# Kernel optimization log

Measured on AMD Instinct MI355X. Metric: run time of the kernel, lower is better.

The kernel has to match this reference:

```python
import jax, jax.numpy as jnp
import numpy as np


def setup_inputs() -> dict:
    key = jax.random.key(0)
    kq, kk, kv = jax.random.split(key, 3)
    B, H, S, D = 1, 16, 4096, 64
    Q = jax.random.normal(kq, (B, H, S, D), dtype=jnp.float32)
    K = jax.random.normal(kk, (B, H, S, D), dtype=jnp.float32)
    V = jax.random.normal(kv, (B, H, S, D), dtype=jnp.float32)
    return {"Q": Q, "K": K, "V": V}


def reference(Q, K, V):
    # scores: [B, H, len_q, len_k], scaled by sqrt(dim_k)
    dim_k = K.shape[-1]
    scale = 1.0 / jnp.sqrt(jnp.asarray(dim_k, dtype=Q.dtype))
    scores = jnp.einsum("bhqd,bhkd->bhqk", Q, K) * scale
    attention = jax.nn.softmax(scores, axis=-1)
    context = jnp.einsum("bhqk,bhkd->bhqd", attention, V)
    return context
```

## Files before the change

kernel.cpp:

```cpp
#include <hip/hip_runtime.h>
#include <hip/hip_bf16.h>

typedef short bf16x8 __attribute__((ext_vector_type(8)));
typedef __bf16 bfv8  __attribute__((ext_vector_type(8)));
typedef __bf16 bfv4  __attribute__((ext_vector_type(4)));
typedef float f32x4  __attribute__((ext_vector_type(4)));

#define S_LEN 4096
#define DDIM  64
#define KVB   32
#define QBLK  128
#define NHEAD 16
#define THR   7.0f
#define VOFFB 4096
#define BUFSZ 9216

#define MFMA(a, b, c) __builtin_amdgcn_mfma_f32_16x16x32_bf16((a), (b), (c), 0, 0, 0)

static __device__ __forceinline__ float exp2v(float x) {
    return __builtin_amdgcn_exp2f(x);
}

static __device__ __forceinline__ int4 cvt8(float4 a, float4 b) {
    bfv8 r;
    r[0] = (__bf16)a.x; r[1] = (__bf16)a.y; r[2] = (__bf16)a.z; r[3] = (__bf16)a.w;
    r[4] = (__bf16)b.x; r[5] = (__bf16)b.y; r[6] = (__bf16)b.z; r[7] = (__bf16)b.w;
    return __builtin_bit_cast(int4, r);
}
static __device__ __forceinline__ int2 cvt4(f32x4 a) {
    bfv4 r;
    r[0] = (__bf16)a[0]; r[1] = (__bf16)a[1]; r[2] = (__bf16)a[2]; r[3] = (__bf16)a[3];
    return __builtin_bit_cast(int2, r);
}

static __device__ __forceinline__ bf16x8 ldfrag(const unsigned char* base, int row, int doff) {
    int addr = (row * 128 + doff * 2) ^ ((row & 7) << 4);
    return *reinterpret_cast<const bf16x8*>(base + addr);
}

static __device__ __forceinline__ void stage(unsigned char* base, int swK, int swV,
                                             float4 ka, float4 kb, int4 vt) {
    *reinterpret_cast<int4*>(base + swK)         = cvt8(ka, kb);
    *reinterpret_cast<int4*>(base + VOFFB + swV) = vt;
}

static __device__ __forceinline__ bf16x8 softmax_pb(f32x4 s0, f32x4 s1, float& m,
                                                    f32x4 acc[4], f32x4& lacc) {
    float mx = fmaxf(fmaxf(fmaxf(s0[0], s0[1]), s0[2]),
                     fmaxf(fmaxf(s0[3], s1[0]),
                           fmaxf(s1[1], fmaxf(s1[2], s1[3]))));
    if (!__all(mx <= m + THR)) {
        float pm = fmaxf(mx, __shfl_xor(mx, 16));
        pm = fmaxf(pm, __shfl_xor(pm, 32));
        float mn = fmaxf(m, pm);
        float al = exp2v(m - mn);
        #pragma unroll
        for (int dk = 0; dk < 4; ++dk)
            #pragma unroll
            for (int j = 0; j < 4; ++j) acc[dk][j] *= al;
        #pragma unroll
        for (int j = 0; j < 4; ++j) lacc[j] *= al;
        m = mn;
    }
    bfv8 r;
    #pragma unroll
    for (int j = 0; j < 4; ++j) {
        r[2 * j]     = (__bf16)exp2v(s0[j] - m);
        r[2 * j + 1] = (__bf16)exp2v(s1[j] - m);
    }
    return __builtin_bit_cast(bf16x8, r);
}

__global__ __launch_bounds__(256) void transpose_v(
    const float* __restrict__ Vg, unsigned short* __restrict__ wsVT)
{
    const int h  = blockIdx.y;
    const int kt = blockIdx.x;
    const int t  = threadIdx.x;
    __shared__ __align__(16) unsigned short vt[32][68];

    {
        const int key = t >> 3;
        const int d0  = (t & 7) * 8;
        const float* vp = Vg + (((size_t)h * S_LEN) + (size_t)kt * 32 + key) * DDIM + d0;
        float4 a = *reinterpret_cast<const float4*>(vp);
        float4 b = *reinterpret_cast<const float4*>(vp + 4);
        int4 w = cvt8(a, b);
        int2 lo = {w.x, w.y}, hi = {w.z, w.w};
        *reinterpret_cast<int2*>(&vt[key][d0])     = lo;
        *reinterpret_cast<int2*>(&vt[key][d0 + 4]) = hi;
    }
    __syncthreads();
    {
        const int d  = t >> 2;
        const int p0 = (t & 3) * 8;
        unsigned short out[8];
        #pragma unroll
        for (int i = 0; i < 8; ++i) {
            int p   = p0 + i;
            int key = 4 * (p >> 3) + ((p & 7) >> 1) + 16 * (p & 1);
            out[i] = vt[key][d];
        }
        size_t off = (((size_t)h * DDIM + d) * 128 + kt) * 32 + p0;
        *reinterpret_cast<int4*>(wsVT + off) = *reinterpret_cast<const int4*>(out);
    }
}

template <int KSPLIT>
__global__ __launch_bounds__(256, 3) void attn_fwd(
    const float* __restrict__ Qg, const float* __restrict__ Kg,
    const unsigned short* __restrict__ wsVT, float* __restrict__ Og,
    unsigned short* __restrict__ wsO, float* __restrict__ wsML)
{
    const int h    = blockIdx.y;
    const int qb   = blockIdx.x;
    const int ks   = (KSPLIT > 1) ? blockIdx.z : 0;
    const int NT   = (S_LEN / KVB) / KSPLIT;
    const int tid  = threadIdx.x;
    const int lane = tid & 63;
    const int wv   = tid >> 6;
    const int g    = lane >> 4;
    const int r16  = lane & 15;

    __shared__ __align__(16) unsigned char lds[2 * BUFSZ];

    const float QSC = 0.125f * 1.44269504088896f;
    const int qrow0 = qb * QBLK + wv * 32 + r16;
    bf16x8 qf0[2], qf1[2];
    {
        const float* qp0 = Qg + ((size_t)h * S_LEN + qrow0) * DDIM;
        const float* qp1 = qp0 + 16 * DDIM;
        #pragma unroll
        for (int c = 0; c < 2; ++c) {
            float4 x = *reinterpret_cast<const float4*>(qp0 + 32 * c + 8 * g);
            float4 y = *reinterpret_cast<const float4*>(qp0 + 32 * c + 8 * g + 4);
            float4 xs = {x.x * QSC, x.y * QSC, x.z * QSC, x.w * QSC};
            float4 ys = {y.x * QSC, y.y * QSC, y.z * QSC, y.w * QSC};
            qf0[c] = __builtin_bit_cast(bf16x8, cvt8(xs, ys));
            x = *reinterpret_cast<const float4*>(qp1 + 32 * c + 8 * g);
            y = *reinterpret_cast<const float4*>(qp1 + 32 * c + 8 * g + 4);
            xs = {x.x * QSC, x.y * QSC, x.z * QSC, x.w * QSC};
            ys = {y.x * QSC, y.y * QSC, y.z * QSC, y.w * QSC};
            qf1[c] = __builtin_bit_cast(bf16x8, cvt8(xs, ys));
        }
    }

    bf16x8 ones;
    #pragma unroll
    for (int e = 0; e < 8; ++e) ones[e] = (short)0x3F80;

    const int srow = tid >> 3;
    const int sd   = (tid & 7) * 8;
    const int swK  = (srow * 128 + sd * 2) ^ ((srow & 7) << 4);
    const int vrow = tid >> 2;
    const int swV  = vrow * 80 + (tid & 3) * 16;

    const float* kp = Kg + (size_t)h * S_LEN * DDIM
                    + (size_t)ks * (S_LEN / KSPLIT) * DDIM
                    + (size_t)srow * DDIM + sd;
    const unsigned short* vtp = wsVT
        + (((size_t)h * DDIM + vrow) * 128 + (size_t)ks * (128 / KSPLIT)) * 32
        + (tid & 3) * 8;

    float4 ka = *reinterpret_cast<const float4*>(kp);
    float4 kb = *reinterpret_cast<const float4*>(kp + 4);
    int4   vt = *reinterpret_cast<const int4*>(vtp);
    stage(lds, swK, swV, ka, kb, vt);
    kp += KVB * DDIM; vtp += 32;
    ka = *reinterpret_cast<const float4*>(kp);
    kb = *reinterpret_cast<const float4*>(kp + 4);
    vt = *reinterpret_cast<const int4*>(vtp);
    __syncthreads();

    const f32x4 z0 = {0.f, 0.f, 0.f, 0.f};
    f32x4 accA[4] = {z0, z0, z0, z0};
    f32x4 accB[4] = {z0, z0, z0, z0};
    f32x4 laccA = z0, laccB = z0;
    float m0 = -INFINITY, m1 = -INFINITY;

    int c = 0;
    for (int kt = 0; kt < NT; ++kt) {
        const unsigned char* Klds = lds + c * BUFSZ;
        const unsigned char* Vlds = Klds + VOFFB;

        if (kt + 1 < NT) {
            stage(lds + (c ^ 1) * BUFSZ, swK, swV, ka, kb, vt);
            if (kt + 2 < NT) {
                kp += KVB * DDIM; vtp += 32;
                ka = *reinterpret_cast<const float4*>(kp);
                kb = *reinterpret_cast<const float4*>(kp + 4);
                vt = *reinterpret_cast<const int4*>(vtp);
            }
        }

        bf16x8 vf[4];
        {
            const unsigned char* vbase = Vlds + r16 * 80 + 16 * g;
            #pragma unroll
            for (int dk = 0; dk < 4; ++dk)
                vf[dk] = *reinterpret_cast<const bf16x8*>(vbase + dk * 1280);
        }

        f32x4 sA0 = z0, sA1 = z0, sB0 = z0, sB1 = z0;
        #pragma unroll
        for (int cc = 0; cc < 2; ++cc) {
            bf16x8 k0 = ldfrag(Klds, r16,      32 * cc + 8 * g);
            bf16x8 k1 = ldfrag(Klds, 16 + r16, 32 * cc + 8 * g);
            sA0 = MFMA(k0, qf0[cc], sA0);
            sA1 = MFMA(k1, qf0[cc], sA1);
            sB0 = MFMA(k0, qf1[cc], sB0);
            sB1 = MFMA(k1, qf1[cc], sB1);
        }

        bf16x8 pbA = softmax_pb(sA0, sA1, m0, accA, laccA);
        bf16x8 pbB = softmax_pb(sB0, sB1, m1, accB, laccB);

        laccA = MFMA(ones, pbA, laccA);
        #pragma unroll
        for (int dk = 0; dk < 4; ++dk) accA[dk] = MFMA(vf[dk], pbA, accA[dk]);
        laccB = MFMA(ones, pbB, laccB);
        #pragma unroll
        for (int dk = 0; dk < 4; ++dk) accB[dk] = MFMA(vf[dk], pbB, accB[dk]);

        __syncthreads();
        c ^= 1;
    }

    if (KSPLIT == 1) {
        float inv0 = 1.0f / laccA[0];
        float* op = Og + ((size_t)h * S_LEN + qrow0) * DDIM;
        #pragma unroll
        for (int dk = 0; dk < 4; ++dk) {
            float4 o = {accA[dk][0] * inv0, accA[dk][1] * inv0,
                        accA[dk][2] * inv0, accA[dk][3] * inv0};
            *reinterpret_cast<float4*>(op + 16 * dk + 4 * g) = o;
        }
        float inv1 = 1.0f / laccB[0];
        op += 16 * DDIM;
        #pragma unroll
        for (int dk = 0; dk < 4; ++dk) {
            float4 o = {accB[dk][0] * inv1, accB[dk][1] * inv1,
                        accB[dk][2] * inv1, accB[dk][3] * inv1};
            *reinterpret_cast<float4*>(op + 16 * dk + 4 * g) = o;
        }
    } else {
        const size_t R0 = (size_t)h * S_LEN + qrow0;
        unsigned short* o0 = wsO + ((size_t)ks * (NHEAD * S_LEN) + R0) * DDIM;
        #pragma unroll
        for (int dk = 0; dk < 4; ++dk)
            *reinterpret_cast<int2*>(o0 + 16 * dk + 4 * g) = cvt4(accA[dk]);
        o0 += 16 * DDIM;
        #pragma unroll
        for (int dk = 0; dk < 4; ++dk)
            *reinterpret_cast<int2*>(o0 + 16 * dk + 4 * g) = cvt4(accB[dk]);
        if (g == 0) {
            float2 v0 = {m0, laccA[0]};
            float2 v1 = {m1, laccB[0]};
            *reinterpret_cast<float2*>(wsML + ((size_t)ks * (NHEAD * S_LEN) + R0) * 2)      = v0;
            *reinterpret_cast<float2*>(wsML + ((size_t)ks * (NHEAD * S_LEN) + R0 + 16) * 2) = v1;
        }
    }
}

__global__ __launch_bounds__(256) void combine2(
    const unsigned short* __restrict__ wsO, const float* __restrict__ wsML,
    float* __restrict__ Og)
{
    const int NR = NHEAD * S_LEN;
    int t  = blockIdx.x * 256 + threadIdx.x;
    int R  = t >> 4;
    int d4 = (t & 15) * 4;
    float2 ml0 = *reinterpret_cast<const float2*>(wsML + (size_t)R * 2);
    float2 ml1 = *reinterpret_cast<const float2*>(wsML + ((size_t)NR + R) * 2);
    float m  = fmaxf(ml0.x, ml1.x);
    float a0 = exp2v(ml0.x - m);
    float a1 = exp2v(ml1.x - m);
    float inv = 1.0f / (a0 * ml0.y + a1 * ml1.y);
    a0 *= inv; a1 *= inv;
    bfv4 o0 = __builtin_bit_cast(bfv4,
        *reinterpret_cast<const int2*>(wsO + (size_t)R * DDIM + d4));
    bfv4 o1 = __builtin_bit_cast(bfv4,
        *reinterpret_cast<const int2*>(wsO + ((size_t)NR + R) * DDIM + d4));
    float4 o = {a0 * (float)o0[0] + a1 * (float)o1[0],
                a0 * (float)o0[1] + a1 * (float)o1[1],
                a0 * (float)o0[2] + a1 * (float)o1[2],
                a0 * (float)o0[3] + a1 * (float)o1[3]};
    *reinterpret_cast<float4*>(Og + (size_t)R * DDIM + d4) = o;
}

extern "C" void kernel_launch(void* const* d_in, const int* in_sizes, int n_in,
                              void* d_out, int out_size, void* d_ws, size_t ws_size,
                              hipStream_t stream) {
    const float* Q = (const float*)d_in[0];
    const float* K = (const float*)d_in[1];
    const float* V = (const float*)d_in[2];
    float* O = (float*)d_out;

    const size_t nVT = (size_t)NHEAD * DDIM * S_LEN;
    const size_t nO  = (size_t)2 * NHEAD * S_LEN * DDIM;
    const size_t nML = (size_t)2 * NHEAD * S_LEN * 2;
    const size_t needVT   = nVT * 2;
    const size_t needFull = nVT * 2 + nO * 2 + nML * 4;

    unsigned short* wsVT = (unsigned short*)d_ws;
    transpose_v<<<dim3(128, NHEAD), dim3(256, 1, 1), 0, stream>>>(V, wsVT);

    if (ws_size >= needFull) {
        unsigned short* wsO  = wsVT + nVT;
        float*          wsML = (float*)(wsO + nO);
        dim3 grid(S_LEN / QBLK, NHEAD, 2);
        attn_fwd<2><<<grid, dim3(256, 1, 1), 0, stream>>>(Q, K, wsVT, O, wsO, wsML);
        int nthr = NHEAD * S_LEN * (DDIM / 4);
        combine2<<<dim3(nthr / 256), dim3(256, 1, 1), 0, stream>>>(wsO, wsML, O);
    } else if (ws_size >= needVT) {
        dim3 grid(S_LEN / QBLK, NHEAD, 1);
        attn_fwd<1><<<grid, dim3(256, 1, 1), 0, stream>>>(Q, K, wsVT, O, nullptr, nullptr);
    }
}
```

Before: 102.7 us.

## Pre-convert K to swizzled bf16 tiles and split keys three ways

K is now converted to bf16 once in a prep kernel and written as pre-swizzled 4KB tiles, so the attention kernel loads one int4 per thread and copies it straight into LDS. Previously every query block reloaded and converted fp32 K. The V transpose layout is also made tile-contiguous. The key split grows from 2 to 3 (43/43/42 tiles) to put more blocks on the device, and the combine kernel is generalized to N splits. The cost is a larger workspace, an extra K pass in the prep kernel, and more partial-output traffic in the combine.

```diff
diff --git a/kernel.cpp b/kernel.cpp
--- a/kernel.cpp
+++ b/kernel.cpp
@@ -38,10 +38,10 @@
     return *reinterpret_cast<const bf16x8*>(base + addr);
 }
 
-static __device__ __forceinline__ void stage(unsigned char* base, int swK, int swV,
-                                             float4 ka, float4 kb, int4 vt) {
-    *reinterpret_cast<int4*>(base + swK)         = cvt8(ka, kb);
-    *reinterpret_cast<int4*>(base + VOFFB + swV) = vt;
+static __device__ __forceinline__ void stage(unsigned char* base, int kdst, int vdst,
+                                             int4 kv, int4 vv) {
+    *reinterpret_cast<int4*>(base + kdst)         = kv;
+    *reinterpret_cast<int4*>(base + VOFFB + vdst) = vv;
 }
 
 static __device__ __forceinline__ bf16x8 softmax_pb(f32x4 s0, f32x4 s1, float& m,
@@ -71,24 +71,33 @@
     return __builtin_bit_cast(bf16x8, r);
 }
 
-__global__ __launch_bounds__(256) void transpose_v(
-    const float* __restrict__ Vg, unsigned short* __restrict__ wsVT)
+__global__ __launch_bounds__(256) void prep(
+    const float* __restrict__ Kg, const float* __restrict__ Vg,
+    unsigned short* __restrict__ wsKT, unsigned short* __restrict__ wsVT)
 {
     const int h  = blockIdx.y;
     const int kt = blockIdx.x;
     const int t  = threadIdx.x;
+    const int srow = t >> 3;
+    const int sd   = (t & 7) * 8;
+    const size_t src = (((size_t)h * S_LEN) + (size_t)kt * 32 + srow) * DDIM + sd;
+
+    {
+        float4 a = *reinterpret_cast<const float4*>(Kg + src);
+        float4 b = *reinterpret_cast<const float4*>(Kg + src + 4);
+        const int swK = (srow * 128 + sd * 2) ^ ((srow & 7) << 4);
+        *reinterpret_cast<int4*>(reinterpret_cast<char*>(wsKT)
+            + ((size_t)(h * 128 + kt) << 12) + swK) = cvt8(a, b);
+    }
+
     __shared__ __align__(16) unsigned short vt[32][68];
-
     {
-        const int key = t >> 3;
-        const int d0  = (t & 7) * 8;
-        const float* vp = Vg + (((size_t)h * S_LEN) + (size_t)kt * 32 + key) * DDIM + d0;
-        float4 a = *reinterpret_cast<const float4*>(vp);
-        float4 b = *reinterpret_cast<const float4*>(vp + 4);
+        float4 a = *reinterpret_cast<const float4*>(Vg + src);
+        float4 b = *reinterpret_cast<const float4*>(Vg + src + 4);
         int4 w = cvt8(a, b);
         int2 lo = {w.x, w.y}, hi = {w.z, w.w};
-        *reinterpret_cast<int2*>(&vt[key][d0])     = lo;
-        *reinterpret_cast<int2*>(&vt[key][d0 + 4]) = hi;
+        *reinterpret_cast<int2*>(&vt[srow][sd])     = lo;
+        *reinterpret_cast<int2*>(&vt[srow][sd + 4]) = hi;
     }
     __syncthreads();
     {
@@ -101,21 +110,24 @@
             int key = 4 * (p >> 3) + ((p & 7) >> 1) + 16 * (p & 1);
             out[i] = vt[key][d];
         }
-        size_t off = (((size_t)h * DDIM + d) * 128 + kt) * 32 + p0;
-        *reinterpret_cast<int4*>(wsVT + off) = *reinterpret_cast<const int4*>(out);
+        *reinterpret_cast<int4*>(wsVT + ((size_t)(h * 128 + kt) * 2048) + d * 32 + p0)
+            = *reinterpret_cast<const int4*>(out);
     }
 }
 
 template <int KSPLIT>
 __global__ __launch_bounds__(256, 3) void attn_fwd(
-    const float* __restrict__ Qg, const float* __restrict__ Kg,
+    const float* __restrict__ Qg, const unsigned short* __restrict__ wsKT,
     const unsigned short* __restrict__ wsVT, float* __restrict__ Og,
     unsigned short* __restrict__ wsO, float* __restrict__ wsML)
 {
     const int h    = blockIdx.y;
     const int qb   = blockIdx.x;
     const int ks   = (KSPLIT > 1) ? blockIdx.z : 0;
-    const int NT   = (S_LEN / KVB) / KSPLIT;
+    int kt0, NT;
+    if (KSPLIT == 3)      { kt0 = ks * 43; NT = (ks < 2) ? 43 : 42; }
+    else if (KSPLIT == 2) { kt0 = ks * 64; NT = 64; }
+    else                  { kt0 = 0;       NT = 128; }
     const int tid  = threadIdx.x;
     const int lane = tid & 63;
     const int wv   = tid >> 6;
@@ -149,27 +161,18 @@
     #pragma unroll
     for (int e = 0; e < 8; ++e) ones[e] = (short)0x3F80;
 
-    const int srow = tid >> 3;
-    const int sd   = (tid & 7) * 8;
-    const int swK  = (srow * 128 + sd * 2) ^ ((srow & 7) << 4);
-    const int vrow = tid >> 2;
-    const int swV  = vrow * 80 + (tid & 3) * 16;
-
-    const float* kp = Kg + (size_t)h * S_LEN * DDIM
-                    + (size_t)ks * (S_LEN / KSPLIT) * DDIM
-                    + (size_t)srow * DDIM + sd;
-    const unsigned short* vtp = wsVT
-        + (((size_t)h * DDIM + vrow) * 128 + (size_t)ks * (128 / KSPLIT)) * 32
-        + (tid & 3) * 8;
-
-    float4 ka = *reinterpret_cast<const float4*>(kp);
-    float4 kb = *reinterpret_cast<const float4*>(kp + 4);
-    int4   vt = *reinterpret_cast<const int4*>(vtp);
-    stage(lds, swK, swV, ka, kb, vt);
-    kp += KVB * DDIM; vtp += 32;
-    ka = *reinterpret_cast<const float4*>(kp);
-    kb = *reinterpret_cast<const float4*>(kp + 4);
-    vt = *reinterpret_cast<const int4*>(vtp);
+    const int kdst = tid * 16;
+    const int vdst = (tid >> 2) * 80 + (tid & 3) * 16;
+    const unsigned short* ktp = wsKT + ((size_t)(h * 128 + kt0) * 2048) + tid * 8;
+    const unsigned short* vtp = wsVT + ((size_t)(h * 128 + kt0) * 2048)
+                              + (tid >> 2) * 32 + (tid & 3) * 8;
+
+    int4 kv = *reinterpret_cast<const int4*>(ktp);
+    int4 vv = *reinterpret_cast<const int4*>(vtp);
+    stage(lds, kdst, vdst, kv, vv);
+    ktp += 2048; vtp += 2048;
+    kv = *reinterpret_cast<const int4*>(ktp);
+    vv = *reinterpret_cast<const int4*>(vtp);
     __syncthreads();
 
     const f32x4 z0 = {0.f, 0.f, 0.f, 0.f};
@@ -184,12 +187,11 @@
         const unsigned char* Vlds = Klds + VOFFB;
 
         if (kt + 1 < NT) {
-            stage(lds + (c ^ 1) * BUFSZ, swK, swV, ka, kb, vt);
+            stage(lds + (c ^ 1) * BUFSZ, kdst, vdst, kv, vv);
             if (kt + 2 < NT) {
-                kp += KVB * DDIM; vtp += 32;
-                ka = *reinterpret_cast<const float4*>(kp);
-                kb = *reinterpret_cast<const float4*>(kp + 4);
-                vt = *reinterpret_cast<const int4*>(vtp);
+                ktp += 2048; vtp += 2048;
+                kv = *reinterpret_cast<const int4*>(ktp);
+                vv = *reinterpret_cast<const int4*>(vtp);
             }
         }
 
@@ -262,7 +264,8 @@
     }
 }
 
-__global__ __launch_bounds__(256) void combine2(
+template <int NS>
+__global__ __launch_bounds__(256) void combineN(
     const unsigned short* __restrict__ wsO, const float* __restrict__ wsML,
     float* __restrict__ Og)
 {
@@ -270,21 +273,26 @@
     int t  = blockIdx.x * 256 + threadIdx.x;
     int R  = t >> 4;
     int d4 = (t & 15) * 4;
-    float2 ml0 = *reinterpret_cast<const float2*>(wsML + (size_t)R * 2);
-    float2 ml1 = *reinterpret_cast<const float2*>(wsML + ((size_t)NR + R) * 2);
-    float m  = fmaxf(ml0.x, ml1.x);
-    float a0 = exp2v(ml0.x - m);
-    float a1 = exp2v(ml1.x - m);
-    float inv = 1.0f / (a0 * ml0.y + a1 * ml1.y);
-    a0 *= inv; a1 *= inv;
-    bfv4 o0 = __builtin_bit_cast(bfv4,
-        *reinterpret_cast<const int2*>(wsO + (size_t)R * DDIM + d4));
-    bfv4 o1 = __builtin_bit_cast(bfv4,
-        *reinterpret_cast<const int2*>(wsO + ((size_t)NR + R) * DDIM + d4));
-    float4 o = {a0 * (float)o0[0] + a1 * (float)o1[0],
-                a0 * (float)o0[1] + a1 * (float)o1[1],
-                a0 * (float)o0[2] + a1 * (float)o1[2],
-                a0 * (float)o0[3] + a1 * (float)o1[3]};
+    float2 ml[NS];
+    float m = -INFINITY;
+    #pragma unroll
+    for (int s = 0; s < NS; ++s) {
+        ml[s] = *reinterpret_cast<const float2*>(wsML + ((size_t)s * NR + R) * 2);
+        m = fmaxf(m, ml[s].x);
+    }
+    float a[NS], den = 0.f;
+    #pragma unroll
+    for (int s = 0; s < NS; ++s) { a[s] = exp2v(ml[s].x - m); den += a[s] * ml[s].y; }
+    float inv = 1.0f / den;
+    float4 o = {0.f, 0.f, 0.f, 0.f};
+    #pragma unroll
+    for (int s = 0; s < NS; ++s) {
+        bfv4 ob = __builtin_bit_cast(bfv4,
+            *reinterpret_cast<const int2*>(wsO + ((size_t)s * NR + R) * DDIM + d4));
+        float w = a[s] * inv;
+        o.x += w * (float)ob[0]; o.y += w * (float)ob[1];
+        o.z += w * (float)ob[2]; o.w += w * (float)ob[3];
+    }
     *reinterpret_cast<float4*>(Og + (size_t)R * DDIM + d4) = o;
 }
 
@@ -296,24 +304,35 @@
     const float* V = (const float*)d_in[2];
     float* O = (float*)d_out;
 
-    const size_t nVT = (size_t)NHEAD * DDIM * S_LEN;
-    const size_t nO  = (size_t)2 * NHEAD * S_LEN * DDIM;
-    const size_t nML = (size_t)2 * NHEAD * S_LEN * 2;
-    const size_t needVT   = nVT * 2;
-    const size_t needFull = nVT * 2 + nO * 2 + nML * 4;
-
-    unsigned short* wsVT = (unsigned short*)d_ws;
-    transpose_v<<<dim3(128, NHEAD), dim3(256, 1, 1), 0, stream>>>(V, wsVT);
-
-    if (ws_size >= needFull) {
-        unsigned short* wsO  = wsVT + nVT;
-        float*          wsML = (float*)(wsO + nO);
+    const size_t nKT = (size_t)NHEAD * 128 * 2048;
+    const size_t nVT = (size_t)NHEAD * 128 * 2048;
+    const size_t nOrow = (size_t)NHEAD * S_LEN * DDIM;
+    const size_t nMLrow = (size_t)NHEAD * S_LEN * 2;
+    const size_t baseB  = (nKT + nVT) * 2;
+    const size_t perSplitB = nOrow * 2 + nMLrow * 4;
+    const size_t need3 = baseB + 3 * perSplitB;
+    const size_t need2 = baseB + 2 * perSplitB;
+
+    unsigned short* wsKT = (unsigned short*)d_ws;
+    unsigned short* wsVT = wsKT + nKT;
+    unsigned short* wsO  = wsVT + nVT;
+
+    prep<<<dim3(128, NHEAD), dim3(256, 1, 1), 0, stream>>>(K, V, wsKT, wsVT);
+
+    if (ws_size >= need3) {
+        float* wsML = (float*)(wsO + 3 * nOrow);
+        dim3 grid(S_LEN / QBLK, NHEAD, 3);
+        attn_fwd<3><<<grid, dim3(256, 1, 1), 0, stream>>>(Q, wsKT, wsVT, O, wsO, wsML);
+        int nthr = NHEAD * S_LEN * (DDIM / 4);
+        combineN<3><<<dim3(nthr / 256), dim3(256, 1, 1), 0, stream>>>(wsO, wsML, O);
+    } else if (ws_size >= need2) {
+        float* wsML = (float*)(wsO + 2 * nOrow);
         dim3 grid(S_LEN / QBLK, NHEAD, 2);
-        attn_fwd<2><<<grid, dim3(256, 1, 1), 0, stream>>>(Q, K, wsVT, O, wsO, wsML);
+        attn_fwd<2><<<grid, dim3(256, 1, 1), 0, stream>>>(Q, wsKT, wsVT, O, wsO, wsML);
         int nthr = NHEAD * S_LEN * (DDIM / 4);
-        combine2<<<dim3(nthr / 256), dim3(256, 1, 1), 0, stream>>>(wsO, wsML, O);
-    } else if (ws_size >= needVT) {
+        combineN<2><<<dim3(nthr / 256), dim3(256, 1, 1), 0, stream>>>(wsO, wsML, O);
+    } else {
         dim3 grid(S_LEN / QBLK, NHEAD, 1);
-        attn_fwd<1><<<grid, dim3(256, 1, 1), 0, stream>>>(Q, K, wsVT, O, nullptr, nullptr);
-    }
-}
+        attn_fwd<1><<<grid, dim3(256, 1, 1), 0, stream>>>(Q, wsKT, wsVT, O, nullptr, nullptr);
+    }
+}
```

After: 103.0 us. About the same (+0.3%).
